# Optimization experiments

Measured on AMD Instinct MI355X. Metric: run time of the kernel, lower is better.

## Reference

```python
import jax, jax.numpy as jnp
import numpy as np

B, T, D = 2, 2048, 1024
H, HD = 16, 64
DL, DC = 512, 256
THETA = 10000.0
LN_EPS = 1e-5


def setup_inputs() -> dict:
    key = jax.random.key(0)
    ks = jax.random.split(key, 8)
    s = 0.02
    return {
        "x": jax.random.normal(ks[0], (B, T, D), jnp.float32),
        "W_q": jax.random.normal(ks[1], (H * HD, D), jnp.float32) * s,
        "b_q": jnp.zeros((H * HD,), jnp.float32),
        "W_kvl": jax.random.normal(ks[2], (DL, D), jnp.float32) * s,
        "b_kvl": jnp.zeros((DL,), jnp.float32),
        "ts_scale": jnp.ones((DL,), jnp.float32),
        "ts_shift": jnp.zeros((DL,), jnp.float32),
        "W_comp": jax.random.normal(ks[3], (DC, DL), jnp.float32) * s,
        "W_exp": jax.random.normal(ks[4], (DL, DC), jnp.float32) * s,
        "ln_g": jnp.ones((DC,), jnp.float32),
        "ln_b": jnp.zeros((DC,), jnp.float32),
        "W_fkv": jax.random.normal(ks[5], (2 * H * HD, DL), jnp.float32) * s,
        "b_fkv": jnp.zeros((2 * H * HD,), jnp.float32),
        "W_out": jax.random.normal(ks[6], (D, H * HD), jnp.float32) * s,
        "b_out": jnp.zeros((D,), jnp.float32),
    }


def _rope_tables(t_len):
    inv_freq = 1.0 / (THETA ** (jnp.arange(0, HD, 2, dtype=jnp.float32) / HD))
    pos = jnp.arange(t_len, dtype=jnp.float32)
    freqs = pos[:, None] * inv_freq[None, :]          # [T, HD/2]
    cos = jnp.concatenate([jnp.cos(freqs)] * 2, -1)   # [T, HD]
    sin = jnp.concatenate([jnp.sin(freqs)] * 2, -1)
    return cos[None, None], sin[None, None]           # [1,1,T,HD]


def _rotate_half(z):
    return jnp.concatenate([-z[..., HD // 2:], z[..., :HD // 2]], -1)


def reference(x, W_q, b_q, W_kvl, b_kvl, ts_scale, ts_shift, W_comp, W_exp,
              ln_g, ln_b, W_fkv, b_fkv, W_out, b_out):
    # Q path: [B,T,D] -> [B,H,T,HD]
    q = (jnp.einsum('btd,ed->bte', x, W_q) + b_q).reshape(B, T, H, HD).transpose(0, 2, 1, 3)

    # KV latent + learned KVSplice bottleneck
    kvl = jnp.einsum('btd,ld->btl', x, W_kvl) + b_kvl                 # [B,T,DL]
    xt = kvl * jax.nn.softplus(ts_scale) + ts_shift
    c = jnp.einsum('btl,cl->btc', xt, W_comp)                         # [B,T,DC]
    mu = jnp.mean(c, -1, keepdims=True)
    var = jnp.mean(jnp.square(c - mu), -1, keepdims=True)
    c = (c - mu) * jax.lax.rsqrt(var + LN_EPS) * ln_g + ln_b
    dec = jnp.einsum('btc,lc->btl', c, W_exp)                         # [B,T,DL]

    # Decompress latent to K,V
    kv = jnp.einsum('btl,el->bte', dec, W_fkv) + b_fkv                # [B,T,2*H*HD]
    kv = kv.reshape(B, T, 2, H, HD).transpose(2, 0, 3, 1, 4)          # [2,B,H,T,HD]
    k, v = kv[0], kv[1]

    # RoPE
    cos, sin = _rope_tables(T)
    q = q * cos + _rotate_half(q) * sin
    k = k * cos + _rotate_half(k) * sin

    # Causal SDPA
    scale = 1.0 / np.sqrt(HD)
    scores = jnp.einsum('bhqd,bhkd->bhqk', q, k) * scale
    mask = jnp.tril(jnp.ones((T, T), bool))
    scores = jnp.where(mask, scores, jnp.float32(-1e30))
    attn = jax.nn.softmax(scores, axis=-1)
    o = jnp.einsum('bhqk,bhkd->bhqd', attn, v)
    o = o.transpose(0, 2, 1, 3).reshape(B, T, H * HD)
    return jnp.einsum('bte,de->btd', o, W_out) + b_out
```

## Files before the change

### kernel.cpp

```cpp
#include <hip/hip_runtime.h>
#include <math.h>

#define B_SZ   2
#define T_SEQ  2048
#define NH     16
#define HDIM   64
#define D_MOD  1024
#define DL     512
#define DC     256
#define MROWS  4096

typedef __attribute__((ext_vector_type(8))) short bf16x8;
typedef __attribute__((ext_vector_type(4))) float f32x4;

#define SCALE_Q 0.18033688011112042f

static __device__ __forceinline__ unsigned short f2bf(float f) {
    union { float f; unsigned u; } v; v.f = f;
    unsigned r = v.u + 0x7fffu + ((v.u >> 16) & 1u);
    return (unsigned short)(r >> 16);
}

static __device__ __forceinline__ void gl_lds16(const unsigned short* g,
                                                unsigned short* l) {
    __builtin_amdgcn_global_load_lds(
        (const __attribute__((address_space(1))) unsigned int*)g,
        (__attribute__((address_space(3))) unsigned int*)l, 16, 0, 0);
}

__global__ __launch_bounds__(256) void cvt_bf16(
    const float* __restrict__ x,  const float* __restrict__ wq,
    const float* __restrict__ wkvl, const float* __restrict__ wcomp,
    const float* __restrict__ wexp, const float* __restrict__ wfkv,
    const float* __restrict__ wout,
    unsigned short* __restrict__ xb,  unsigned short* __restrict__ wqh,
    unsigned short* __restrict__ wkvlh, unsigned short* __restrict__ wcomph,
    unsigned short* __restrict__ wexph, unsigned short* __restrict__ wfkvh,
    unsigned short* __restrict__ wouth, float2* __restrict__ rope_tab)
{
    const int g = blockIdx.x * 256 + threadIdx.x;
    const int stride = gridDim.x * 256;
#define CVT_SEG(src, dst, n4)                                              \
    for (int i = g; i < (n4); i += stride) {                               \
        float4 v = ((const float4*)(src))[i];                              \
        unsigned short h[4] = {f2bf(v.x), f2bf(v.y), f2bf(v.z), f2bf(v.w)};\
        *(uint2*)((dst) + (size_t)i * 4) = *(uint2*)h;                     \
    }
    CVT_SEG(x, xb, 1048576)
    CVT_SEG(wq, wqh, 262144)
    CVT_SEG(wkvl, wkvlh, 131072)
    CVT_SEG(wcomp, wcomph, 32768)
    CVT_SEG(wexp, wexph, 32768)
    CVT_SEG(wfkv, wfkvh, 262144)
    CVT_SEG(wout, wouth, 262144)
#undef CVT_SEG
    for (int i = g; i < T_SEQ * 32; i += stride) {
        const int t = i >> 5, fi = i & 31;
        const float inv = __expf((float)fi * (-9.210340371976184f / 32.0f));
        float sn, cs; sincosf((float)t * inv, &sn, &cs);
        rope_tab[i] = make_float2(cs, sn);
    }
}

#define GEMM64x128_PROLOG(Aptr, Wptr, Kdim)                                    \
    __shared__ unsigned short As[64 * 32];                                     \
    __shared__ unsigned short Ws[128 * 32];                                    \
    const int tid = threadIdx.x;                                               \
    const int w = tid >> 6, lane = tid & 63;                                   \
    const int l16 = lane & 15, quad = lane >> 4;                               \
    const int wm = w >> 1, wn = w & 1;                                         \
    const int srow = lane >> 2, scol = (lane & 3) << 3;                        \
    const unsigned short* Ag = (Aptr) + (size_t)(m0 + w * 16 + srow) * (Kdim) + scol; \
    const unsigned short* Wg = (Wptr) + (size_t)(n0 + w * 32 + srow) * (Kdim) + scol; \
    unsigned short* Al  = &As[w * 512];                                        \
    unsigned short* Wl0 = &Ws[w * 1024];                                       \
    unsigned short* Wl1 = &Ws[w * 1024 + 512];                                 \
    f32x4 acc[2][4];                                                           \
    _Pragma("unroll") for (int i = 0; i < 2; ++i)                              \
        _Pragma("unroll") for (int j = 0; j < 4; ++j)                          \
            acc[i][j] = (f32x4){0.f, 0.f, 0.f, 0.f};                           \
    for (int k0 = 0; k0 < (Kdim); k0 += 32) {                                  \
        __syncthreads();                                                       \
        gl_lds16(Ag + k0, Al);                                                 \
        gl_lds16(Wg + k0, Wl0);                                                \
        gl_lds16(Wg + (size_t)16 * (Kdim) + k0, Wl1);                          \
        __syncthreads();                                                       \
        bf16x8 af[2], bfr[4];                                                  \
        _Pragma("unroll") for (int i = 0; i < 2; ++i)                          \
            af[i] = *(const bf16x8*)&As[(wm * 32 + i * 16 + l16) * 32 + quad * 8]; \
        _Pragma("unroll") for (int j = 0; j < 4; ++j)                          \
            bfr[j] = *(const bf16x8*)&Ws[(wn * 64 + j * 16 + l16) * 32 + quad * 8]; \
        _Pragma("unroll") for (int i = 0; i < 2; ++i)                          \
            _Pragma("unroll") for (int j = 0; j < 4; ++j)                      \
                acc[i][j] = __builtin_amdgcn_mfma_f32_16x16x32_bf16(           \
                    af[i], bfr[j], acc[i][j], 0, 0, 0);                        \
    }

__global__ __launch_bounds__(256) void gemm_qxt(
    const unsigned short* __restrict__ A, const unsigned short* __restrict__ Wq,
    const unsigned short* __restrict__ Wkvl,
    const float* __restrict__ b_q, const float* __restrict__ b_kvl,
    const float* __restrict__ ts_scale, const float* __restrict__ ts_shift,
    const float2* __restrict__ tab,
    unsigned short* __restrict__ qh, unsigned short* __restrict__ xt)
{
    const int m0 = blockIdx.x * 64;
    const bool is_q = (blockIdx.y < 8);
    const int n0 = is_q ? blockIdx.y * 128 : (blockIdx.y - 8) * 128;
    const unsigned short* W = is_q ? Wq : Wkvl;

    GEMM64x128_PROLOG(A, W, D_MOD)

    if (is_q) {
#pragma unroll
        for (int i = 0; i < 2; ++i) {
#pragma unroll
            for (int j = 0; j < 4; ++j) {
                const int col = n0 + wn * 64 + j * 16 + l16;
                const int h = col >> 6, hd = col & 63;
                const float bv = b_q[col];
                const float bvp = b_q[col ^ 32];
                const float sgn = (hd < 32) ? -1.f : 1.f;
#pragma unroll
                for (int reg = 0; reg < 4; ++reg) {
                    const int row = m0 + wm * 32 + i * 16 + quad * 4 + reg;
                    const int b = row >> 11, t = row & (T_SEQ - 1);
                    const float2 cssn = tab[t * 32 + (hd & 31)];
                    const float v  = acc[i][j][reg] + bv;
                    const float vp = acc[i][j ^ 2][reg] + bvp;
                    const float r = (v * cssn.x + sgn * vp * cssn.y) * SCALE_Q;
                    qh[(((size_t)b * NH + h) * T_SEQ + t) * HDIM + hd] = f2bf(r);
                }
            }
        }
    } else {
#pragma unroll
        for (int i = 0; i < 2; ++i) {
#pragma unroll
            for (int j = 0; j < 4; ++j) {
                const int col = n0 + wn * 64 + j * 16 + l16;
                const float bv = b_kvl[col];
                const float sp_s = log1pf(expf(ts_scale[col]));
                const float sp_t = ts_shift[col];
#pragma unroll
                for (int reg = 0; reg < 4; ++reg) {
                    const int row = m0 + wm * 32 + i * 16 + quad * 4 + reg;
                    const float val = (acc[i][j][reg] + bv) * sp_s + sp_t;
                    xt[(size_t)row * DL + col] = f2bf(val);
                }
            }
        }
    }
}

__global__ __launch_bounds__(256) void gemm_kv(
    const unsigned short* __restrict__ A, const unsigned short* __restrict__ W,
    const float* __restrict__ bias, const float2* __restrict__ tab,
    unsigned short* __restrict__ kh, unsigned short* __restrict__ vth)
{
    const int m0 = blockIdx.x * 64, n0 = blockIdx.y * 128;

    GEMM64x128_PROLOG(A, W, DL)

    if (n0 < 1024) {
#pragma unroll
        for (int i = 0; i < 2; ++i) {
#pragma unroll
            for (int j = 0; j < 4; ++j) {
                const int col = n0 + wn * 64 + j * 16 + l16;
                const int h = (col >> 6) & 15, hd = col & 63;
                const float bv = bias[col];
                const float bvp = bias[col ^ 32];
                const float sgn = (hd < 32) ? -1.f : 1.f;
#pragma unroll
                for (int reg = 0; reg < 4; ++reg) {
                    const int row = m0 + wm * 32 + i * 16 + quad * 4 + reg;
                    const int b = row >> 11, t = row & (T_SEQ - 1);
                    const float2 cssn = tab[t * 32 + (hd & 31)];
                    const float v  = acc[i][j][reg] + bv;
                    const float vp = acc[i][j ^ 2][reg] + bvp;
                    const float r = v * cssn.x + sgn * vp * cssn.y;
                    kh[(((size_t)b * NH + h) * T_SEQ + t) * HDIM + hd] = f2bf(r);
                }
            }
        }
    } else {
#pragma unroll
        for (int i = 0; i < 2; ++i) {
#pragma unroll
            for (int j = 0; j < 4; ++j) {
                const int col = n0 + wn * 64 + j * 16 + l16;
                const int cv = col - 1024;
                const int h = cv >> 6, hd = cv & 63;
                const float bv = bias[col];
                unsigned short hv[4];
                const int r0 = m0 + wm * 32 + i * 16 + quad * 4;
                const int b = r0 >> 11, t0 = r0 & (T_SEQ - 1);
#pragma unroll
                for (int reg = 0; reg < 4; ++reg)
                    hv[reg] = f2bf(acc[i][j][reg] + bv);
                *(uint2*)&vth[(((size_t)b * NH + h) * HDIM + hd) * T_SEQ + t0] =
                    *(uint2*)hv;
            }
        }
    }
}

__global__ __launch_bounds__(256) void gemm_out(
    const unsigned short* __restrict__ A, const unsigned short* __restrict__ W,
    const float* __restrict__ bias, float* __restrict__ C)
{
    const int m0 = blockIdx.x * 64, n0 = blockIdx.y * 128;

    GEMM64x128_PROLOG(A, W, D_MOD)

#pragma unroll
    for (int i = 0; i < 2; ++i)
#pragma unroll
        for (int j = 0; j < 4; ++j) {
            const int col = n0 + wn * 64 + j * 16 + l16;
            const float bv = bias[col];
#pragma unroll
            for (int reg = 0; reg < 4; ++reg) {
                const int row = m0 + wm * 32 + i * 16 + quad * 4 + reg;
                C[(size_t)row * D_MOD + col] = acc[i][j][reg] + bv;
            }
        }
}

enum { EP_C = 0, EP_B = 1 };

template <int EPI>
__global__ __launch_bounds__(256) void gemm_mfma64(
    const unsigned short* __restrict__ A, const unsigned short* __restrict__ W,
    void* __restrict__ Cv, int N, int K)
{
    __shared__ unsigned short As[64 * 32];
    __shared__ unsigned short Ws[64 * 32];

    const int tid = threadIdx.x;
    const int w = tid >> 6, lane = tid & 63;
    const int l16 = lane & 15, quad = lane >> 4;
    const int wm = w >> 1, wn = w & 1;
    const int m0 = blockIdx.x * 64, n0 = blockIdx.y * 64;

    const unsigned short* Ag = A + (size_t)(m0 + w * 16 + (lane >> 2)) * K + ((lane & 3) << 3);
    const unsigned short* Wg = W + (size_t)(n0 + w * 16 + (lane >> 2)) * K + ((lane & 3) << 3);
    unsigned short* Al = &As[w * 512];
    unsigned short* Wl = &Ws[w * 512];

    f32x4 acc[2][2];
#pragma unroll
    for (int i = 0; i < 2; ++i)
#pragma unroll
        for (int j = 0; j < 2; ++j) acc[i][j] = (f32x4){0.f, 0.f, 0.f, 0.f};

    for (int k0 = 0; k0 < K; k0 += 32) {
        __syncthreads();
        gl_lds16(Ag + k0, Al);
        gl_lds16(Wg + k0, Wl);
        __syncthreads();

        bf16x8 af[2], bfr[2];
#pragma unroll
        for (int i = 0; i < 2; ++i)
            af[i] = *(const bf16x8*)&As[(wm * 32 + i * 16 + l16) * 32 + quad * 8];
#pragma unroll
        for (int j = 0; j < 2; ++j)
            bfr[j] = *(const bf16x8*)&Ws[(wn * 32 + j * 16 + l16) * 32 + quad * 8];
#pragma unroll
        for (int i = 0; i < 2; ++i)
#pragma unroll
            for (int j = 0; j < 2; ++j)
                acc[i][j] = __builtin_amdgcn_mfma_f32_16x16x32_bf16(
                    af[i], bfr[j], acc[i][j], 0, 0, 0);
    }

#pragma unroll
    for (int i = 0; i < 2; ++i) {
#pragma unroll
        for (int j = 0; j < 2; ++j) {
            const int col = n0 + wn * 32 + j * 16 + l16;
#pragma unroll
            for (int reg = 0; reg < 4; ++reg) {
                const int row = m0 + wm * 32 + i * 16 + quad * 4 + reg;
                if (EPI == EP_C)
                    ((float*)Cv)[(size_t)row * N + col] = acc[i][j][reg];
                else
                    ((unsigned short*)Cv)[(size_t)row * N + col] = f2bf(acc[i][j][reg]);
            }
        }
    }
}

__global__ __launch_bounds__(256) void ln_rows(const float* __restrict__ cbuf,
                                               unsigned short* __restrict__ outb,
                                               const float* __restrict__ g,
                                               const float* __restrict__ bta)
{
    const int row = blockIdx.x, tid = threadIdx.x;
    float v = cbuf[(size_t)row * DC + tid];
    __shared__ float red[8];

    float s = v;
#pragma unroll
    for (int off = 32; off > 0; off >>= 1) s += __shfl_down(s, off);
    if ((tid & 63) == 0) red[tid >> 6] = s;
    __syncthreads();
    const float mu = (red[0] + red[1] + red[2] + red[3]) * (1.0f / DC);

    const float d = v - mu;
    float s2 = d * d;
#pragma unroll
    for (int off = 32; off > 0; off >>= 1) s2 += __shfl_down(s2, off);
    if ((tid & 63) == 0) red[4 + (tid >> 6)] = s2;
    __syncthreads();
    const float var = (red[4] + red[5] + red[6] + red[7]) * (1.0f / DC);

    outb[(size_t)row * DC + tid] = f2bf(d * rsqrtf(var + 1e-5f) * g[tid] + bta[tid]);
}

__global__ __launch_bounds__(128) void flash_mfma(
    const unsigned short* __restrict__ q, const unsigned short* __restrict__ k,
    const unsigned short* __restrict__ vt, unsigned short* __restrict__ o)
{
    __shared__ unsigned short Ks[64 * 72];
    __shared__ unsigned short Vs[64 * 72];
    __shared__ unsigned short Ps[64 * 72];

    const int bh = blockIdx.x & 31;
    const int j  = 31 - (blockIdx.x >> 5);
    const int q0 = j * 64;
    const int tid = threadIdx.x;
    const int w = tid >> 6, lane = tid & 63;
    const int l16 = lane & 15, quad = lane >> 4;

    bf16x8 qf[2][2];
#pragma unroll
    for (int mt = 0; mt < 2; ++mt)
#pragma unroll
        for (int kk = 0; kk < 2; ++kk)
            qf[mt][kk] = *(const bf16x8*)(q +
                ((size_t)bh * T_SEQ + q0 + w * 32 + mt * 16 + l16) * HDIM + kk * 32 + quad * 8);

    f32x4 of[2][4];
    float lrow[2][4];
#pragma unroll
    for (int mt = 0; mt < 2; ++mt) {
#pragma unroll
        for (int dt = 0; dt < 4; ++dt) of[mt][dt] = (f32x4){0.f, 0.f, 0.f, 0.f};
#pragma unroll
        for (int r = 0; r < 4; ++r) lrow[mt][r] = 0.f;
    }

    const int ldr = tid >> 1;
    const int ldc = (tid & 1) * 32;
    const unsigned short* kgb = k + ((size_t)bh * T_SEQ + ldr) * HDIM + ldc;
    const unsigned short* vgb = vt + ((size_t)bh * HDIM + ldr) * T_SEQ + ldc;

    const int kend = (j + 1) * 64;
    for (int k0 = 0; k0 < kend; k0 += 64) {
        __syncthreads();
        {
            const unsigned short* kg = kgb + (size_t)k0 * HDIM;
            *(bf16x8*)&Ks[ldr * 72 + ldc]      = *(const bf16x8*)kg;
            *(bf16x8*)&Ks[ldr * 72 + ldc + 8]  = *(const bf16x8*)(kg + 8);
            *(bf16x8*)&Ks[ldr * 72 + ldc + 16] = *(const bf16x8*)(kg + 16);
            *(bf16x8*)&Ks[ldr * 72 + ldc + 24] = *(const bf16x8*)(kg + 24);
            const unsigned short* vg = vgb + k0;
            *(bf16x8*)&Vs[ldr * 72 + ldc]      = *(const bf16x8*)vg;
            *(bf16x8*)&Vs[ldr * 72 + ldc + 8]  = *(const bf16x8*)(vg + 8);
            *(bf16x8*)&Vs[ldr * 72 + ldc + 16] = *(const bf16x8*)(vg + 16);
            *(bf16x8*)&Vs[ldr * 72 + ldc + 24] = *(const bf16x8*)(vg + 24);
        }
        __syncthreads();

        bf16x8 kf[4][2];
#pragma unroll
        for (int nt = 0; nt < 4; ++nt)
#pragma unroll
            for (int kk = 0; kk < 2; ++kk)
                kf[nt][kk] = *(const bf16x8*)&Ks[(nt * 16 + l16) * 72 + kk * 32 + quad * 8];

#pragma unroll
        for (int mt = 0; mt < 2; ++mt) {
            const int rbase = q0 + w * 32 + mt * 16;
            f32x4 sf[4];
#pragma unroll
            for (int nt = 0; nt < 4; ++nt) {
                sf[nt] = (f32x4){0.f, 0.f, 0.f, 0.f};
#pragma unroll
                for (int kk = 0; kk < 2; ++kk)
                    sf[nt] = __builtin_amdgcn_mfma_f32_16x16x32_bf16(qf[mt][kk], kf[nt][kk], sf[nt], 0, 0, 0);
            }
            const bool need_mask = (k0 + 63) > rbase;
#pragma unroll
            for (int reg = 0; reg < 4; ++reg) {
                float a0 = sf[0][reg], a1 = sf[1][reg], a2 = sf[2][reg], a3 = sf[3][reg];
                if (need_mask) {
                    const int tq = rbase + quad * 4 + reg;
                    if (k0 +      l16 > tq) a0 = -1e30f;
                    if (k0 + 16 + l16 > tq) a1 = -1e30f;
                    if (k0 + 32 + l16 > tq) a2 = -1e30f;
                    if (k0 + 48 + l16 > tq) a3 = -1e30f;
                }
                union { float f; unsigned u; } u0, u1, u2, u3;
                u0.f = exp2f(a0); u1.f = exp2f(a1);
                u2.f = exp2f(a2); u3.f = exp2f(a3);
                const int prow = (w * 32 + mt * 16 + quad * 4 + reg) * 72 + l16;
                Ps[prow]      = (unsigned short)(u0.u >> 16);
                Ps[prow + 16] = (unsigned short)(u1.u >> 16);
                Ps[prow + 32] = (unsigned short)(u2.u >> 16);
                Ps[prow + 48] = (unsigned short)(u3.u >> 16);
                u0.u &= 0xffff0000u; u1.u &= 0xffff0000u;
                u2.u &= 0xffff0000u; u3.u &= 0xffff0000u;
                lrow[mt][reg] += (u0.f + u1.f) + (u2.f + u3.f);
            }
        }

        bf16x8 vf[4][2];
#pragma unroll
        for (int dt = 0; dt < 4; ++dt)
#pragma unroll
            for (int kk = 0; kk < 2; ++kk)
                vf[dt][kk] = *(const bf16x8*)&Vs[(dt * 16 + l16) * 72 + kk * 32 + quad * 8];

#pragma unroll
        for (int mt = 0; mt < 2; ++mt) {
            bf16x8 pf[2];
#pragma unroll
            for (int kk = 0; kk < 2; ++kk)
                pf[kk] = *(const bf16x8*)&Ps[(w * 32 + mt * 16 + l16) * 72 + kk * 32 + quad * 8];
#pragma unroll
            for (int dt = 0; dt < 4; ++dt)
#pragma unroll
                for (int kk = 0; kk < 2; ++kk)
                    of[mt][dt] = __builtin_amdgcn_mfma_f32_16x16x32_bf16(pf[kk], vf[dt][kk], of[mt][dt], 0, 0, 0);
        }
    }

    const int b = bh >> 4, h = bh & 15;
#pragma unroll
    for (int mt = 0; mt < 2; ++mt) {
        const int rbase = q0 + w * 32 + mt * 16;
#pragma unroll
        for (int reg = 0; reg < 4; ++reg) {
            float l = lrow[mt][reg];
            l += __shfl_xor(l, 1);
            l += __shfl_xor(l, 2);
            l += __shfl_xor(l, 4);
            l += __shfl_xor(l, 8);
            const float inv = 1.0f / l;
            const int t = rbase + quad * 4 + reg;
#pragma unroll
            for (int dt = 0; dt < 4; ++dt)
                o[((size_t)b * T_SEQ + t) * (NH * HDIM) + h * HDIM + dt * 16 + l16] =
                    f2bf(of[mt][dt][reg] * inv);
        }
    }
}

extern "C" void kernel_launch(void* const* d_in, const int* in_sizes, int n_in,
                              void* d_out, int out_size, void* d_ws, size_t ws_size,
                              hipStream_t stream)
{
    (void)in_sizes; (void)n_in; (void)out_size; (void)ws_size;

    const float* x        = (const float*)d_in[0];
    const float* W_q      = (const float*)d_in[1];
    const float* b_q      = (const float*)d_in[2];
    const float* W_kvl    = (const float*)d_in[3];
    const float* b_kvl    = (const float*)d_in[4];
    const float* ts_scale = (const float*)d_in[5];
    const float* ts_shift = (const float*)d_in[6];
    const float* W_comp   = (const float*)d_in[7];
    const float* W_exp    = (const float*)d_in[8];
    const float* ln_g     = (const float*)d_in[9];
    const float* ln_b     = (const float*)d_in[10];
    const float* W_fkv    = (const float*)d_in[11];
    const float* b_fkv    = (const float*)d_in[12];
    const float* W_out    = (const float*)d_in[13];
    const float* b_out    = (const float*)d_in[14];
    float* out = (float*)d_out;

    char* p = (char*)d_ws;
    unsigned short* xb     = (unsigned short*)p;             p += 8  * 1024 * 1024;
    unsigned short* wqh    = (unsigned short*)p;             p += 2  * 1024 * 1024;
    unsigned short* wkvlh  = (unsigned short*)p;             p += 1  * 1024 * 1024;
    unsigned short* wcomph = (unsigned short*)p;             p += 256 * 1024;
    unsigned short* wexph  = (unsigned short*)p;             p += 256 * 1024;
    unsigned short* wfkvh  = (unsigned short*)p;             p += 2  * 1024 * 1024;
    unsigned short* wouth  = (unsigned short*)p;             p += 2  * 1024 * 1024;
    unsigned short* qh     = (unsigned short*)p;             p += 8  * 1024 * 1024;
    unsigned short* kh     = (unsigned short*)p;             p += 8  * 1024 * 1024;
    unsigned short* vth    = (unsigned short*)p;             p += 8  * 1024 * 1024;
    unsigned short* xt     = (unsigned short*)p;             p += 4  * 1024 * 1024;
    float*          cb     = (float*)p;                      p += 4  * 1024 * 1024;
    unsigned short* cbh    = (unsigned short*)p;             p += 2  * 1024 * 1024;
    unsigned short* dec    = (unsigned short*)p;             p += 4  * 1024 * 1024;
    unsigned short* ob     = (unsigned short*)p;             p += 8  * 1024 * 1024;
    float2*         tab    = (float2*)p;                     p += 512 * 1024;

    const dim3 blk(256);

    cvt_bf16<<<1024, blk, 0, stream>>>(x, W_q, W_kvl, W_comp, W_exp, W_fkv, W_out,
                                       xb, wqh, wkvlh, wcomph, wexph, wfkvh, wouth,
                                       tab);

    gemm_qxt<<<dim3(64, 12), blk, 0, stream>>>(
        xb, wqh, wkvlh, b_q, b_kvl, ts_scale, ts_shift, tab, qh, xt);

    gemm_mfma64<EP_C><<<dim3(64, 4), blk, 0, stream>>>(
        xt, wcomph, cb, DC, DL);

    ln_rows<<<MROWS, blk, 0, stream>>>(cb, cbh, ln_g, ln_b);

    gemm_mfma64<EP_B><<<dim3(64, 8), blk, 0, stream>>>(
        cbh, wexph, dec, DL, DC);

    gemm_kv<<<dim3(64, 16), blk, 0, stream>>>(
        dec, wfkvh, b_fkv, tab, kh, vth);

    flash_mfma<<<1024, dim3(128), 0, stream>>>(qh, kh, vth, ob);

    gemm_out<<<dim3(64, 8), blk, 0, stream>>>(
        ob, wouth, b_out, out);
}
```

Measured before the change: 252.2 us.

## Fuse compression GEMM with LayerNorm and enlarge flash attention query tile

Replaces the fp32 compression GEMM plus separate LayerNorm kernel with one kernel in which each block computes 16 full rows of 256 columns and applies LayerNorm in registers, using a single-pass sum and sum-of-squares. This removes the fp32 intermediate round trip and one launch. Flash attention now uses 256 threads and 128-row query tiles with 512 blocks, so each K/V tile load is shared by twice as many queries. In exchange the fused GEMM has a narrow M tile and uses the less stable E[x^2]-mu^2 variance, and the causal diagonal now spans two key tiles per block.

```diff
diff --git a/kernel.cpp b/kernel.cpp
--- a/kernel.cpp
+++ b/kernel.cpp
@@ -228,12 +228,89 @@
         }
 }
 
-enum { EP_C = 0, EP_B = 1 };
-
-template <int EPI>
-__global__ __launch_bounds__(256) void gemm_mfma64(
+__global__ __launch_bounds__(256) void gemm_c_ln(
     const unsigned short* __restrict__ A, const unsigned short* __restrict__ W,
-    void* __restrict__ Cv, int N, int K)
+    const float* __restrict__ g, const float* __restrict__ bta,
+    unsigned short* __restrict__ outb)
+{
+    __shared__ unsigned short As[16 * 32];
+    __shared__ unsigned short Ws[256 * 32];
+    __shared__ float redS[4][16];
+    __shared__ float redQ[4][16];
+
+    const int tid = threadIdx.x;
+    const int w = tid >> 6, lane = tid & 63;
+    const int l16 = lane & 15, quad = lane >> 4;
+    const int m0 = blockIdx.x * 16;
+
+    const int srow = lane >> 2, scol = (lane & 3) << 3;
+    const unsigned short* Ag = A + (size_t)(m0 + srow) * DL + scol;
+    const unsigned short* Wg = W + (size_t)(w * 64 + srow) * DL + scol;
+
+    f32x4 acc[4];
+#pragma unroll
+    for (int j = 0; j < 4; ++j) acc[j] = (f32x4){0.f, 0.f, 0.f, 0.f};
+
+    for (int k0 = 0; k0 < DL; k0 += 32) {
+        __syncthreads();
+        if (w == 0) gl_lds16(Ag + k0, &As[0]);
+#pragma unroll
+        for (int c = 0; c < 4; ++c)
+            gl_lds16(Wg + (size_t)(c * 16) * DL + k0, &Ws[(w * 64 + c * 16) * 32]);
+        __syncthreads();
+
+        const bf16x8 af = *(const bf16x8*)&As[l16 * 32 + quad * 8];
+        bf16x8 bfr[4];
+#pragma unroll
+        for (int j = 0; j < 4; ++j)
+            bfr[j] = *(const bf16x8*)&Ws[(w * 64 + j * 16 + l16) * 32 + quad * 8];
+#pragma unroll
+        for (int j = 0; j < 4; ++j)
+            acc[j] = __builtin_amdgcn_mfma_f32_16x16x32_bf16(af, bfr[j], acc[j], 0, 0, 0);
+    }
+
+    float s[4], q2[4];
+#pragma unroll
+    for (int reg = 0; reg < 4; ++reg) {
+        float sv = (acc[0][reg] + acc[1][reg]) + (acc[2][reg] + acc[3][reg]);
+        float qv = (acc[0][reg] * acc[0][reg] + acc[1][reg] * acc[1][reg]) +
+                   (acc[2][reg] * acc[2][reg] + acc[3][reg] * acc[3][reg]);
+#pragma unroll
+        for (int off = 1; off < 16; off <<= 1) {
+            sv += __shfl_xor(sv, off);
+            qv += __shfl_xor(qv, off);
+        }
+        s[reg] = sv; q2[reg] = qv;
+    }
+    if (l16 == 0) {
+#pragma unroll
+        for (int reg = 0; reg < 4; ++reg) {
+            redS[w][quad * 4 + reg] = s[reg];
+            redQ[w][quad * 4 + reg] = q2[reg];
+        }
+    }
+    __syncthreads();
+
+#pragma unroll
+    for (int reg = 0; reg < 4; ++reg) {
+        const int r = quad * 4 + reg;
+        const float sum = (redS[0][r] + redS[1][r]) + (redS[2][r] + redS[3][r]);
+        const float sq  = (redQ[0][r] + redQ[1][r]) + (redQ[2][r] + redQ[3][r]);
+        const float mu  = sum * (1.0f / DC);
+        const float var = sq * (1.0f / DC) - mu * mu;
+        const float rstd = rsqrtf(var + 1e-5f);
+#pragma unroll
+        for (int j = 0; j < 4; ++j) {
+            const int col = w * 64 + j * 16 + l16;
+            const float val = (acc[j][reg] - mu) * rstd * g[col] + bta[col];
+            outb[(size_t)(m0 + r) * DC + col] = f2bf(val);
+        }
+    }
+}
+
+__global__ __launch_bounds__(256) void gemm_mfma64_b(
+    const unsigned short* __restrict__ A, const unsigned short* __restrict__ W,
+    unsigned short* __restrict__ Cv, int N, int K)
 {
     __shared__ unsigned short As[64 * 32];
     __shared__ unsigned short Ws[64 * 32];
@@ -284,53 +361,23 @@
 #pragma unroll
             for (int reg = 0; reg < 4; ++reg) {
                 const int row = m0 + wm * 32 + i * 16 + quad * 4 + reg;
-                if (EPI == EP_C)
-                    ((float*)Cv)[(size_t)row * N + col] = acc[i][j][reg];
-                else
-                    ((unsigned short*)Cv)[(size_t)row * N + col] = f2bf(acc[i][j][reg]);
-            }
-        }
-    }
-}
-
-__global__ __launch_bounds__(256) void ln_rows(const float* __restrict__ cbuf,
-                                               unsigned short* __restrict__ outb,
-                                               const float* __restrict__ g,
-                                               const float* __restrict__ bta)
-{
-    const int row = blockIdx.x, tid = threadIdx.x;
-    float v = cbuf[(size_t)row * DC + tid];
-    __shared__ float red[8];
-
-    float s = v;
-#pragma unroll
-    for (int off = 32; off > 0; off >>= 1) s += __shfl_down(s, off);
-    if ((tid & 63) == 0) red[tid >> 6] = s;
-    __syncthreads();
-    const float mu = (red[0] + red[1] + red[2] + red[3]) * (1.0f / DC);
-
-    const float d = v - mu;
-    float s2 = d * d;
-#pragma unroll
-    for (int off = 32; off > 0; off >>= 1) s2 += __shfl_down(s2, off);
-    if ((tid & 63) == 0) red[4 + (tid >> 6)] = s2;
-    __syncthreads();
-    const float var = (red[4] + red[5] + red[6] + red[7]) * (1.0f / DC);
-
-    outb[(size_t)row * DC + tid] = f2bf(d * rsqrtf(var + 1e-5f) * g[tid] + bta[tid]);
-}
-
-__global__ __launch_bounds__(128) void flash_mfma(
+                Cv[(size_t)row * N + col] = f2bf(acc[i][j][reg]);
+            }
+        }
+    }
+}
+
+__global__ __launch_bounds__(256, 3) void flash_mfma(
     const unsigned short* __restrict__ q, const unsigned short* __restrict__ k,
     const unsigned short* __restrict__ vt, unsigned short* __restrict__ o)
 {
     __shared__ unsigned short Ks[64 * 72];
     __shared__ unsigned short Vs[64 * 72];
-    __shared__ unsigned short Ps[64 * 72];
+    __shared__ unsigned short Ps[128 * 72];
 
     const int bh = blockIdx.x & 31;
-    const int j  = 31 - (blockIdx.x >> 5);
-    const int q0 = j * 64;
+    const int j  = 15 - (blockIdx.x >> 5);
+    const int q0 = j * 128;
     const int tid = threadIdx.x;
     const int w = tid >> 6, lane = tid & 63;
     const int l16 = lane & 15, quad = lane >> 4;
@@ -353,25 +400,21 @@
         for (int r = 0; r < 4; ++r) lrow[mt][r] = 0.f;
     }
 
-    const int ldr = tid >> 1;
-    const int ldc = (tid & 1) * 32;
+    const int ldr = tid >> 2;
+    const int ldc = (tid & 3) * 16;
     const unsigned short* kgb = k + ((size_t)bh * T_SEQ + ldr) * HDIM + ldc;
     const unsigned short* vgb = vt + ((size_t)bh * HDIM + ldr) * T_SEQ + ldc;
 
-    const int kend = (j + 1) * 64;
+    const int kend = q0 + 128;
     for (int k0 = 0; k0 < kend; k0 += 64) {
         __syncthreads();
         {
             const unsigned short* kg = kgb + (size_t)k0 * HDIM;
-            *(bf16x8*)&Ks[ldr * 72 + ldc]      = *(const bf16x8*)kg;
-            *(bf16x8*)&Ks[ldr * 72 + ldc + 8]  = *(const bf16x8*)(kg + 8);
-            *(bf16x8*)&Ks[ldr * 72 + ldc + 16] = *(const bf16x8*)(kg + 16);
-            *(bf16x8*)&Ks[ldr * 72 + ldc + 24] = *(const bf16x8*)(kg + 24);
+            *(bf16x8*)&Ks[ldr * 72 + ldc]     = *(const bf16x8*)kg;
+            *(bf16x8*)&Ks[ldr * 72 + ldc + 8] = *(const bf16x8*)(kg + 8);
             const unsigned short* vg = vgb + k0;
-            *(bf16x8*)&Vs[ldr * 72 + ldc]      = *(const bf16x8*)vg;
-            *(bf16x8*)&Vs[ldr * 72 + ldc + 8]  = *(const bf16x8*)(vg + 8);
-            *(bf16x8*)&Vs[ldr * 72 + ldc + 16] = *(const bf16x8*)(vg + 16);
-            *(bf16x8*)&Vs[ldr * 72 + ldc + 24] = *(const bf16x8*)(vg + 24);
+            *(bf16x8*)&Vs[ldr * 72 + ldc]     = *(const bf16x8*)vg;
+            *(bf16x8*)&Vs[ldr * 72 + ldc + 8] = *(const bf16x8*)(vg + 8);
         }
         __syncthreads();
 
@@ -495,7 +538,6 @@
     unsigned short* kh     = (unsigned short*)p;             p += 8  * 1024 * 1024;
     unsigned short* vth    = (unsigned short*)p;             p += 8  * 1024 * 1024;
     unsigned short* xt     = (unsigned short*)p;             p += 4  * 1024 * 1024;
-    float*          cb     = (float*)p;                      p += 4  * 1024 * 1024;
     unsigned short* cbh    = (unsigned short*)p;             p += 2  * 1024 * 1024;
     unsigned short* dec    = (unsigned short*)p;             p += 4  * 1024 * 1024;
     unsigned short* ob     = (unsigned short*)p;             p += 8  * 1024 * 1024;
@@ -510,18 +552,16 @@
     gemm_qxt<<<dim3(64, 12), blk, 0, stream>>>(
         xb, wqh, wkvlh, b_q, b_kvl, ts_scale, ts_shift, tab, qh, xt);
 
-    gemm_mfma64<EP_C><<<dim3(64, 4), blk, 0, stream>>>(
-        xt, wcomph, cb, DC, DL);
-
-    ln_rows<<<MROWS, blk, 0, stream>>>(cb, cbh, ln_g, ln_b);
-
-    gemm_mfma64<EP_B><<<dim3(64, 8), blk, 0, stream>>>(
+    gemm_c_ln<<<256, blk, 0, stream>>>(
+        xt, wcomph, ln_g, ln_b, cbh);
+
+    gemm_mfma64_b<<<dim3(64, 8), blk, 0, stream>>>(
         cbh, wexph, dec, DL, DC);
 
     gemm_kv<<<dim3(64, 16), blk, 0, stream>>>(
         dec, wfkvh, b_fkv, tab, kh, vth);
 
-    flash_mfma<<<1024, dim3(128), 0, stream>>>(qh, kh, vth, ob);
+    flash_mfma<<<512, blk, 0, stream>>>(qh, kh, vth, ob);
 
     gemm_out<<<dim3(64, 8), blk, 0, stream>>>(
         ob, wouth, b_out, out);
```

New measurement: 248.3 us. Within noise of the previous version (-1.5%).
